# Performance work log

Measured on AMD Instinct MI355X. Metric: run time of the kernel, lower is better.

Reference implementation:

```python
import jax, jax.numpy as jnp
import numpy as np

DIM = 512
DIM_HEAD = 32
HEADS = DIM // DIM_HEAD
WS = 8  # window (partition) size
INNER = (DIM * 4 * 2 // 3 // 32) * 32  # gated-MLP inner dim = 2720
EPS = 1e-6
LS_INIT = 1e-5


def _ln(x, g, b):
    mu = jnp.mean(x, axis=-1, keepdims=True)
    var = jnp.var(x, axis=-1, keepdims=True)
    return (x - mu) * jax.lax.rsqrt(var + EPS) * g + b


def setup_inputs() -> dict:
    key = jax.random.key(0)
    ks = jax.random.split(key, 8)
    B, H, W = 8, 96, 96
    s = lambda d: 1.0 / np.sqrt(d)
    return {
        "x": jax.random.normal(ks[0], (B, H, W, DIM), jnp.float32),
        "norm1_g": jnp.ones((DIM,), jnp.float32),
        "norm1_b": jnp.zeros((DIM,), jnp.float32),
        "qkv_w": jax.random.normal(ks[1], (DIM, 3 * DIM), jnp.float32) * s(DIM),
        "qkv_b": jnp.zeros((3 * DIM,), jnp.float32),
        "proj_w": jax.random.normal(ks[2], (DIM, DIM), jnp.float32) * s(DIM),
        "proj_b": jnp.zeros((DIM,), jnp.float32),
        "ls1": jnp.full((DIM,), LS_INIT, jnp.float32),
        "norm2_g": jnp.ones((DIM,), jnp.float32),
        "norm2_b": jnp.zeros((DIM,), jnp.float32),
        "glu_w": jax.random.normal(ks[3], (DIM, 2 * INNER), jnp.float32) * s(DIM),
        "glu_b": jnp.zeros((2 * INNER,), jnp.float32),
        "fc2_w": jax.random.normal(ks[4], (INNER, DIM), jnp.float32) * s(INNER),
        "fc2_b": jnp.zeros((DIM,), jnp.float32),
        "ls2": jnp.full((DIM,), LS_INIT, jnp.float32),
    }


def reference(x, norm1_g, norm1_b, qkv_w, qkv_b, proj_w, proj_b, ls1,
              norm2_g, norm2_b, glu_w, glu_b, fc2_w, fc2_b, ls2):
    B, H, W, C = x.shape
    nH, nW = H // WS, W // WS
    T = WS * WS  # tokens per window

    # ---- window attention branch ----
    y = _ln(x, norm1_g, norm1_b)
    # window_partition: (B,H,W,C) -> (B*nH*nW, T, C)
    y = y.reshape(B, nH, WS, nW, WS, C).transpose(0, 1, 3, 2, 4, 5)
    y = y.reshape(-1, T, C)
    qkv = y @ qkv_w + qkv_b                      # (M, T, 3C)
    qkv = qkv.reshape(-1, T, 3, HEADS, DIM_HEAD)
    q, k, v = qkv[:, :, 0], qkv[:, :, 1], qkv[:, :, 2]   # (M, T, h, d)
    scale = DIM_HEAD ** -0.5
    attn = jnp.einsum('mqhd,mkhd->mhqk', q, k) * scale
    attn = jax.nn.softmax(attn, axis=-1)
    o = jnp.einsum('mhqk,mkhd->mqhd', attn, v).reshape(-1, T, C)
    o = o @ proj_w + proj_b
    # window_reverse: (M, T, C) -> (B, H, W, C)
    o = o.reshape(B, nH, nW, WS, WS, C).transpose(0, 1, 3, 2, 4, 5)
    o = o.reshape(B, H, W, C)
    x = x + ls1 * o

    # ---- gated MLP branch (GLU with SiLU) ----
    y = _ln(x, norm2_g, norm2_b)
    h = y @ glu_w + glu_b
    h, gate = jnp.split(h, 2, axis=-1)
    h = h * jax.nn.silu(gate)
    h = h @ fc2_w + fc2_b
    x = x + ls2 * h
    return x
```

## Files before the change

### kernel.cpp

```cpp
#include <hip/hip_runtime.h>
#include <hip/hip_bf16.h>
#include <stdint.h>
#include <math.h>

#define DIM 512
#define INNER 1344
#define INNERP 1408

typedef __attribute__((ext_vector_type(8))) short vbf8;
typedef __attribute__((ext_vector_type(4))) float vf4;
typedef __attribute__((ext_vector_type(4))) int v4i;
typedef __attribute__((ext_vector_type(8))) int v8i;

typedef __attribute__((address_space(1))) void as1void;
typedef __attribute__((address_space(3))) void as3void;

union frag8 {
  v8i w;
  v4i h[2];
};

__device__ __forceinline__ unsigned pk4fp8(float a, float b, float c, float d) {
  int v = __builtin_amdgcn_cvt_pk_fp8_f32(a, b, 0, false);
  v = __builtin_amdgcn_cvt_pk_fp8_f32(c, d, v, true);
  return (unsigned)v;
}

__device__ __forceinline__ uint32_t quant4(float v) {
  uint32_t s = (__float_as_uint(v) >> 31) << 3;
  float a = fabsf(v);
  uint32_t m = (a > 0.25f) + (a > 0.75f) + (a > 1.25f) + (a > 1.75f) +
               (a > 2.5f) + (a > 3.5f) + (a > 5.0f);
  return s | m;
}

#define MFMA_M(a, b, c, sb) \
  __builtin_amdgcn_mfma_scale_f32_16x16x128_f8f6f4((a), (b), (c), 0, 4, 0, 127, 0, (sb))

__global__ void k_transpose4(const float* __restrict__ Wsrc, uint8_t* __restrict__ WT,
                             uint8_t* __restrict__ Wsc, int K, int N, int ldB, int ldS,
                             int nsplit) {
  __shared__ float tile[32][33];
  const int tx = threadIdx.x, ty = threadIdx.y;
  const int n0 = blockIdx.x * 32, k0 = blockIdx.y * 32;
#pragma unroll
  for (int i = 0; i < 32; i += 8) {
    int k = k0 + ty + i, n = n0 + tx;
    if (k < K && n < N) tile[ty + i][tx] = Wsrc[(size_t)k * N + n];
  }
  __syncthreads();
  if (tx < 16) {
#pragma unroll
    for (int i = 0; i < 32; i += 8) {
      int n = n0 + ty + i;
      if (n >= N) continue;
      float v0 = tile[2 * tx][ty + i], v1 = tile[2 * tx + 1][ty + i];
      float m = fmaxf(fabsf(v0), fabsf(v1));
      m = fmaxf(m, __shfl_xor(m, 1));
      m = fmaxf(m, __shfl_xor(m, 2));
      m = fmaxf(m, __shfl_xor(m, 4));
      m = fmaxf(m, __shfl_xor(m, 8));
      uint8_t sbyte;
      float s;
      if (m < 1e-20f) {
        sbyte = 0;
        s = 0.0f;
      } else {
        int e = (int)ceilf(log2f(m * 0.166666672f));
        e = e < -126 ? -126 : (e > 126 ? 126 : e);
        sbyte = (uint8_t)(e + 127);
        s = exp2f((float)(-e));
      }
      int np = n + (n >= nsplit ? 64 : 0);
      WT[(size_t)np * ldB + (k0 >> 1) + tx] =
          (uint8_t)(quant4(v0 * s) | (quant4(v1 * s) << 4));
      if (tx == 0) Wsc[(size_t)np * ldS + (k0 >> 5)] = sbyte;
    }
  }
}

__global__ void k_padbias(const float* __restrict__ b, float* __restrict__ o) {
  int c = blockIdx.x * 256 + threadIdx.x;
  if (c < INNER) o[c] = b[c];
  else if (c >= INNERP && c < INNERP + INNER) o[c] = b[c - 64];
  else if (c < 2816) o[c] = 0.0f;
}

template <bool PART, bool BF16IN>
__global__ __launch_bounds__(256) void k_ln(const void* __restrict__ xin,
                                            const float* __restrict__ gw,
                                            const float* __restrict__ bw,
                                            uint8_t* __restrict__ y) {
  const int wave = threadIdx.x >> 6, lane = threadIdx.x & 63;
  const int tok = blockIdx.x * 4 + wave;
  float vals[8];
  if (BF16IN) {
    const __hip_bfloat16* xr = (const __hip_bfloat16*)xin + (size_t)tok * DIM + lane * 8;
    union {
      vbf8 v;
      ushort e[8];
    } u;
    u.v = *(const vbf8*)xr;
#pragma unroll
    for (int j = 0; j < 8; ++j) vals[j] = __uint_as_float((unsigned)u.e[j] << 16);
  } else {
    const float* xr = (const float*)xin + (size_t)tok * DIM + lane * 8;
    const float4 v0 = *(const float4*)xr;
    const float4 v1 = *(const float4*)(xr + 4);
    vals[0] = v0.x; vals[1] = v0.y; vals[2] = v0.z; vals[3] = v0.w;
    vals[4] = v1.x; vals[5] = v1.y; vals[6] = v1.z; vals[7] = v1.w;
  }
  float s = 0.f, ss = 0.f;
#pragma unroll
  for (int j = 0; j < 8; ++j) {
    s += vals[j];
    ss += vals[j] * vals[j];
  }
#pragma unroll
  for (int off = 32; off > 0; off >>= 1) {
    s += __shfl_xor(s, off);
    ss += __shfl_xor(ss, off);
  }
  const float mu = s * (1.0f / DIM);
  const float rs = rsqrtf(ss * (1.0f / DIM) - mu * mu + 1e-6f);
  size_t orow;
  if (PART) {
    int b = tok / 9216, rem = tok % 9216;
    int h = rem / 96, w = rem % 96;
    orow = (size_t)(((b * 12 + (h >> 3)) * 12 + (w >> 3)) * 64 + (h & 7) * 8 + (w & 7));
  } else {
    orow = (size_t)tok;
  }
  const float4 g0 = *(const float4*)(gw + lane * 8);
  const float4 g1 = *(const float4*)(gw + lane * 8 + 4);
  const float4 b0 = *(const float4*)(bw + lane * 8);
  const float4 b1 = *(const float4*)(bw + lane * 8 + 4);
  const float gg[8] = {g0.x, g0.y, g0.z, g0.w, g1.x, g1.y, g1.z, g1.w};
  const float bb[8] = {b0.x, b0.y, b0.z, b0.w, b1.x, b1.y, b1.z, b1.w};
  float r[8];
#pragma unroll
  for (int j = 0; j < 8; ++j) r[j] = (vals[j] - mu) * rs * gg[j] + bb[j];
  uint2 po;
  po.x = pk4fp8(r[0], r[1], r[2], r[3]);
  po.y = pk4fp8(r[4], r[5], r[6], r[7]);
  *(uint2*)(y + orow * DIM + lane * 8) = po;
}

template <int ROWS>
__device__ __forceinline__ void stage8(const uint8_t* __restrict__ g, int ldKb, char* lds,
                                       int wave, int lane) {
  constexpr int RPW = ROWS / 4;
  const int r0 = wave * RPW;
  const int ro = lane >> 3;
  const int pb = lane & 7;
  const uint8_t* src = g + (size_t)(r0 + ro) * (size_t)ldKb + ((pb ^ ro) << 4);
  char* dst = lds + r0 * 128;
#pragma unroll
  for (int c = 0; c < RPW; c += 8)
    __builtin_amdgcn_global_load_lds((const as1void*)(src + (size_t)c * (size_t)ldKb),
                                     (as3void*)(dst + c * 128), 16, 0, 0);
}
__device__ __forceinline__ v8i fragA8(const char* base, int row, int g) {
  const int ro = row & 7;
  const v4i lo = *(const v4i*)(base + row * 128 + (((2 * g) ^ ro) << 4));
  const v4i hi = *(const v4i*)(base + row * 128 + (((2 * g + 1) ^ ro) << 4));
  return __builtin_shufflevector(lo, hi, 0, 1, 2, 3, 4, 5, 6, 7);
}

template <int ROWS>
__device__ __forceinline__ void stage4(const uint8_t* __restrict__ g, int ldKb, char* lds,
                                       int wave, int lane) {
  constexpr int RPW = ROWS / 4;
  const int r0 = wave * RPW;
  const int srw = lane >> 2, sbk = lane & 3;
  const int fsw = (srw + (srw >> 2)) & 3;
  const uint8_t* src = g + (size_t)(r0 + srw) * (size_t)ldKb + ((sbk ^ fsw) << 4);
  char* dst = lds + r0 * 64;
#pragma unroll
  for (int c = 0; c < RPW; c += 16)
    __builtin_amdgcn_global_load_lds((const as1void*)(src + (size_t)c * (size_t)ldKb),
                                     (as3void*)(dst + c * 64), 16, 0, 0);
}
__device__ __forceinline__ v4i fragB4(const char* base, int row, int g) {
  const int f = (row + (row >> 2)) & 3;
  return *(const v4i*)(base + row * 64 + ((g ^ f) << 4));
}

template <int MODE, int NT>
__global__ __launch_bounds__(256, 2) void k_gemm_m(const uint8_t* __restrict__ A8,
                                                   const uint8_t* __restrict__ B4,
                                                   const uint8_t* __restrict__ Bsc,
                                                   const float* __restrict__ bias,
                                                   void* __restrict__ outp,
                                                   const void* __restrict__ resid,
                                                   const float* __restrict__ lsv, const int K,
                                                   const int ldOut) {
  __shared__ alignas(16) char As[128 * 128];
  __shared__ alignas(16) char Bs[128 * 64];
  const int nwg = gridDim.x;
  int bid = blockIdx.x;
  bid = (bid & 7) * (nwg >> 3) + (bid >> 3);
  const int bm = bid / NT, bn = bid % NT;
  const int tid = threadIdx.x, wave = tid >> 6, lane = tid & 63;
  const int wr = wave >> 1, wc = wave & 1;
  const int cl = lane & 15, g = lane >> 4;
  const int KB = K >> 5, nkt = K >> 7;

  const uint8_t* Ab = A8 + (size_t)bm * 128 * K;
  const uint8_t* Bb = B4 + (size_t)bn * 128 * (K >> 1);

  const uint8_t* bscp[4];
#pragma unroll
  for (int i = 0; i < 4; ++i)
    bscp[i] = Bsc + (size_t)(bn * 128 + wc * 64 + cl + i * 16) * KB + g;

  frag8 bfr[4];
#pragma unroll
  for (int i = 0; i < 4; ++i) bfr[i].w = (v8i){0, 0, 0, 0, 0, 0, 0, 0};
  vf4 acc[4][4] = {};

  for (int t = 0; t < nkt; ++t) {
    __syncthreads();
    stage8<128>(Ab + t * 128, K, As, wave, lane);
    stage4<128>(Bb + t * 64, K >> 1, Bs, wave, lane);
    __syncthreads();
    int sb[4];
#pragma unroll
    for (int i = 0; i < 4; ++i) sb[i] = (int)bscp[i][t * 4];
    v8i af[4];
#pragma unroll
    for (int i = 0; i < 4; ++i) {
      af[i] = fragA8(As, wr * 64 + cl + i * 16, g);
      bfr[i].h[0] = fragB4(Bs, wc * 64 + cl + i * 16, g);
    }
#pragma unroll
    for (int mi = 0; mi < 4; ++mi)
#pragma unroll
      for (int ni = 0; ni < 4; ++ni)
        acc[mi][ni] = MFMA_M(af[mi], bfr[ni].w, acc[mi][ni], sb[ni]);
  }

  const int rl = g << 2;
  const int rbase = bm * 128 + wr * 64;
  const int cbase = bn * 128 + wc * 64;
#pragma unroll
  for (int mi = 0; mi < 4; ++mi) {
#pragma unroll
    for (int j = 0; j < 4; ++j) {
      const int r = rbase + mi * 16 + rl + j;
      size_t orow;
      if (MODE == 1) {
        int m = r >> 6, t = r & 63;
        int b = m / 144, mm = m % 144;
        int wh = mm / 12, ww = mm % 12;
        int h = wh * 8 + (t >> 3), w = ww * 8 + (t & 7);
        orow = (size_t)((b * 96 + h) * 96 + w);
      } else {
        orow = (size_t)r;
      }
#pragma unroll
      for (int ni = 0; ni < 4; ++ni) {
        const int c = cbase + ni * 16 + cl;
        const float v = acc[mi][ni][j] + bias[c];
        if (MODE == 0) {
          ((__hip_bfloat16*)outp)[(size_t)r * ldOut + c] = __float2bfloat16(v);
        } else if (MODE == 1) {
          const float* rx = (const float*)resid;
          ((__hip_bfloat16*)outp)[orow * DIM + c] =
              __float2bfloat16(rx[orow * DIM + c] + lsv[c] * v);
        } else {
          const __hip_bfloat16* rx = (const __hip_bfloat16*)resid;
          ((float*)outp)[(size_t)r * DIM + c] =
              __bfloat162float(rx[(size_t)r * DIM + c]) + lsv[c] * v;
        }
      }
    }
  }
}

__global__ __launch_bounds__(256, 2) void k_gemm_glu_m(const uint8_t* __restrict__ A8,
                                                       const uint8_t* __restrict__ B4,
                                                       const uint8_t* __restrict__ Bsc,
                                                       const float* __restrict__ bias,
                                                       uint8_t* __restrict__ hout) {
  __shared__ alignas(16) char As[128 * 128];
  __shared__ alignas(16) char B0s[64 * 64];
  __shared__ alignas(16) char B1s[64 * 64];
  const int K = DIM, KB = 16;
  const int nwg = gridDim.x;
  int bid = blockIdx.x;
  bid = (bid & 7) * (nwg >> 3) + (bid >> 3);
  const int bm = bid / 22, bn = bid % 22;
  const int tid = threadIdx.x, wave = tid >> 6, lane = tid & 63;
  const int wr = wave >> 1, wc = wave & 1;
  const int cl = lane & 15, g = lane >> 4;

  const uint8_t* Ab = A8 + (size_t)bm * 128 * K;
  const uint8_t* Bb0 = B4 + (size_t)(bn * 64) * 256;
  const uint8_t* Bb1 = B4 + (size_t)(INNERP + bn * 64) * 256;

  const uint8_t* b0scp[2];
  const uint8_t* b1scp[2];
#pragma unroll
  for (int i = 0; i < 2; ++i) {
    int rb = wc * 32 + cl + i * 16;
    b0scp[i] = Bsc + (size_t)(bn * 64 + rb) * KB + g;
    b1scp[i] = Bsc + (size_t)(INNERP + bn * 64 + rb) * KB + g;
  }

  frag8 b0f[2], b1f[2];
#pragma unroll
  for (int i = 0; i < 2; ++i) {
    b0f[i].w = (v8i){0, 0, 0, 0, 0, 0, 0, 0};
    b1f[i].w = (v8i){0, 0, 0, 0, 0, 0, 0, 0};
  }
  vf4 a0[4][2] = {}, a1[4][2] = {};

#pragma unroll
  for (int t = 0; t < 4; ++t) {
    __syncthreads();
    stage8<128>(Ab + t * 128, K, As, wave, lane);
    stage4<64>(Bb0 + t * 64, 256, B0s, wave, lane);
    stage4<64>(Bb1 + t * 64, 256, B1s, wave, lane);
    __syncthreads();
    int sb0[2], sb1[2];
#pragma unroll
    for (int i = 0; i < 2; ++i) {
      sb0[i] = (int)b0scp[i][t * 4];
      sb1[i] = (int)b1scp[i][t * 4];
    }
    v8i af[4];
#pragma unroll
    for (int i = 0; i < 4; ++i) af[i] = fragA8(As, wr * 64 + cl + i * 16, g);
#pragma unroll
    for (int i = 0; i < 2; ++i) {
      b0f[i].h[0] = fragB4(B0s, wc * 32 + cl + i * 16, g);
      b1f[i].h[0] = fragB4(B1s, wc * 32 + cl + i * 16, g);
    }
#pragma unroll
    for (int mi = 0; mi < 4; ++mi)
#pragma unroll
      for (int ni = 0; ni < 2; ++ni) {
        a0[mi][ni] = MFMA_M(af[mi], b0f[ni].w, a0[mi][ni], sb0[ni]);
        a1[mi][ni] = MFMA_M(af[mi], b1f[ni].w, a1[mi][ni], sb1[ni]);
      }
  }

  const int rl = g << 2;
  const int rbase = bm * 128 + wr * 64;
  const int cbase = bn * 64 + wc * 32;
#pragma unroll
  for (int mi = 0; mi < 4; ++mi)
#pragma unroll
    for (int j = 0; j < 4; ++j) {
      const int r = rbase + mi * 16 + rl + j;
#pragma unroll
      for (int ni = 0; ni < 2; ++ni) {
        const int c = cbase + ni * 16 + cl;
        const float a = a0[mi][ni][j] + bias[c];
        const float gv = a1[mi][ni][j] + bias[INNERP + c];
        const float sg = 1.0f / (1.0f + __expf(-gv));
        const float hv = a * gv * sg;
        hout[(size_t)r * INNERP + c] =
            (uint8_t)(__builtin_amdgcn_cvt_pk_fp8_f32(hv, hv, 0, false) & 0xff);
      }
    }
}

__global__ __launch_bounds__(256, 2) void k_attn_mfma(const __hip_bfloat16* __restrict__ qkv,
                                                      uint8_t* __restrict__ o) {
  __shared__ __hip_bfloat16 sm[4][6912];
  const int wave = threadIdx.x >> 6, lane = threadIdx.x & 63;
  const int task = blockIdx.x * 4 + wave;
  const int w = task >> 4, hd = task & 15;
  const int g = lane >> 4, c = lane & 15;
  __hip_bfloat16* smp = sm[wave];
  __hip_bfloat16* smv = smp + 4608;

  const __hip_bfloat16* base = qkv + (size_t)w * 64 * 1536 + hd * 32;

  vbf8 qf[4], kf[4];
#pragma unroll
  for (int i = 0; i < 4; ++i) {
    const __hip_bfloat16* qrow = base + (size_t)(i * 16 + c) * 1536 + g * 8;
    qf[i] = *(const vbf8*)qrow;
    kf[i] = *(const vbf8*)(qrow + 512);
  }

  {
    const __hip_bfloat16* vrow = base + (size_t)lane * 1536 + 1024;
    union {
      vbf8 v;
      ushort e[8];
    } uv[4];
#pragma unroll
    for (int i = 0; i < 4; ++i) uv[i].v = *(const vbf8*)(vrow + i * 8);
#pragma unroll
    for (int d = 0; d < 32; ++d)
      ((ushort*)smv)[d * 72 + lane] = uv[d >> 3].e[d & 7];
  }

  vf4 st[4][4];
#pragma unroll
  for (int iq = 0; iq < 4; ++iq)
#pragma unroll
    for (int it = 0; it < 4; ++it) {
      vf4 z = {};
      st[iq][it] = __builtin_amdgcn_mfma_f32_16x16x32_bf16(qf[iq], kf[it], z, 0, 0, 0);
    }

  float inv[4][4];
#pragma unroll
  for (int iq = 0; iq < 4; ++iq) {
#pragma unroll
    for (int j = 0; j < 4; ++j) {
      float m = fmaxf(fmaxf(st[iq][0][j], st[iq][1][j]), fmaxf(st[iq][2][j], st[iq][3][j]));
      m = fmaxf(m, __shfl_xor(m, 1));
      m = fmaxf(m, __shfl_xor(m, 2));
      m = fmaxf(m, __shfl_xor(m, 4));
      m = fmaxf(m, __shfl_xor(m, 8));
      float s = 0.f;
#pragma unroll
      for (int it = 0; it < 4; ++it) {
        const float e = __expf((st[iq][it][j] - m) * 0.17677669529663687f);
        st[iq][it][j] = e;
        s += e;
      }
      s += __shfl_xor(s, 1);
      s += __shfl_xor(s, 2);
      s += __shfl_xor(s, 4);
      s += __shfl_xor(s, 8);
      inv[iq][j] = 1.0f / s;
    }
  }

#pragma unroll
  for (int iq = 0; iq < 4; ++iq)
#pragma unroll
    for (int j = 0; j < 4; ++j) {
      const int q = iq * 16 + g * 4 + j;
#pragma unroll
      for (int it = 0; it < 4; ++it)
        smp[q * 72 + it * 16 + c] = __float2bfloat16(st[iq][it][j]);
    }

  vf4 ot[4][2] = {};
#pragma unroll
  for (int ks = 0; ks < 2; ++ks) {
    vbf8 pf[4], vfr[2];
#pragma unroll
    for (int iq = 0; iq < 4; ++iq)
      pf[iq] = *(const vbf8*)(smp + (iq * 16 + c) * 72 + ks * 32 + g * 8);
#pragma unroll
    for (int dt = 0; dt < 2; ++dt)
      vfr[dt] = *(const vbf8*)(smv + (dt * 16 + c) * 72 + ks * 32 + g * 8);
#pragma unroll
    for (int iq = 0; iq < 4; ++iq)
#pragma unroll
      for (int dt = 0; dt < 2; ++dt)
        ot[iq][dt] = __builtin_amdgcn_mfma_f32_16x16x32_bf16(pf[iq], vfr[dt], ot[iq][dt], 0, 0, 0);
  }

#pragma unroll
  for (int iq = 0; iq < 4; ++iq)
#pragma unroll
    for (int dt = 0; dt < 2; ++dt)
#pragma unroll
      for (int j = 0; j < 4; ++j) {
        const int q = iq * 16 + g * 4 + j;
        smp[q * 72 + dt * 16 + c] = __float2bfloat16(ot[iq][dt][j] * inv[iq][j]);
      }
  uint8_t* ob = o + (size_t)w * 64 * 512 + hd * 32;
#pragma unroll
  for (int i = 0; i < 4; ++i) {
    const int idx = i * 64 + lane;
    const int row = idx >> 2, chunk = idx & 3;
    union {
      vbf8 v;
      ushort e[8];
    } u;
    u.v = *(const vbf8*)(smp + row * 72 + chunk * 8);
    float f[8];
#pragma unroll
    for (int j = 0; j < 8; ++j) f[j] = __uint_as_float((unsigned)u.e[j] << 16);
    uint2 pv;
    pv.x = pk4fp8(f[0], f[1], f[2], f[3]);
    pv.y = pk4fp8(f[4], f[5], f[6], f[7]);
    *(uint2*)(ob + (size_t)row * 512 + chunk * 8) = pv;
  }
}

extern "C" void kernel_launch(void* const* d_in, const int* in_sizes, int n_in, void* d_out,
                              int out_size, void* d_ws, size_t ws_size, hipStream_t stream) {
  const float* x = (const float*)d_in[0];
  const float* n1g = (const float*)d_in[1];
  const float* n1b = (const float*)d_in[2];
  const float* qkv_w = (const float*)d_in[3];
  const float* qkv_b = (const float*)d_in[4];
  const float* proj_w = (const float*)d_in[5];
  const float* proj_b = (const float*)d_in[6];
  const float* ls1 = (const float*)d_in[7];
  const float* n2g = (const float*)d_in[8];
  const float* n2b = (const float*)d_in[9];
  const float* glu_w = (const float*)d_in[10];
  const float* glu_b = (const float*)d_in[11];
  const float* fc2_w = (const float*)d_in[12];
  const float* fc2_b = (const float*)d_in[13];
  const float* ls2 = (const float*)d_in[14];

  if (ws_size < 268000000u) return;

  char* ws = (char*)d_ws;
  uint8_t* wTq4 = (uint8_t*)(ws + 0);
  uint8_t* wTp4 = (uint8_t*)(ws + 393216);
  uint8_t* wTg4 = (uint8_t*)(ws + 524288);
  uint8_t* wTf4 = (uint8_t*)(ws + 1245184);
  uint8_t* sq = (uint8_t*)(ws + 1605632);
  uint8_t* sp = (uint8_t*)(ws + 1630208);
  uint8_t* sg = (uint8_t*)(ws + 1638400);
  uint8_t* sf = (uint8_t*)(ws + 1683456);
  float* gbias = (float*)(ws + 1705984);
  uint8_t* act8 = (uint8_t*)(ws + 2097152);
  char* big = ws + 39845888;
  __hip_bfloat16* qkvbuf = (__hip_bfloat16*)big;
  uint8_t* h8 = (uint8_t*)big;
  __hip_bfloat16* x1b = (__hip_bfloat16*)(big + 109051904);

  hipMemsetAsync(wTg4, 0, 720896, stream);
  hipMemsetAsync(wTf4, 0, 360448, stream);
  hipMemsetAsync(sg, 0, 45056, stream);
  hipMemsetAsync(sf, 0, 22528, stream);

  dim3 tb(32, 8);
  k_transpose4<<<dim3(48, 16), tb, 0, stream>>>(qkv_w, wTq4, sq, 512, 1536, 256, 16, 1 << 30);
  k_transpose4<<<dim3(16, 16), tb, 0, stream>>>(proj_w, wTp4, sp, 512, 512, 256, 16, 1 << 30);
  k_transpose4<<<dim3(84, 16), tb, 0, stream>>>(glu_w, wTg4, sg, 512, 2688, 256, 16, INNER);
  k_transpose4<<<dim3(16, 42), tb, 0, stream>>>(fc2_w, wTf4, sf, 1344, 512, 704, 44, 1 << 30);
  k_padbias<<<11, 256, 0, stream>>>(glu_b, gbias);

  k_ln<true, false><<<18432, 256, 0, stream>>>(x, n1g, n1b, act8);
  k_gemm_m<0, 12><<<6912, 256, 0, stream>>>(act8, wTq4, sq, qkv_b, qkvbuf, nullptr, nullptr, 512, 1536);
  k_attn_mfma<<<4608, 256, 0, stream>>>(qkvbuf, act8);
  k_gemm_m<1, 4><<<2304, 256, 0, stream>>>(act8, wTp4, sp, proj_b, (void*)x1b, x, ls1, 512, 512);
  k_ln<false, true><<<18432, 256, 0, stream>>>(x1b, n2g, n2b, act8);
  k_gemm_glu_m<<<12672, 256, 0, stream>>>(act8, wTg4, sg, gbias, h8);
  k_gemm_m<2, 4><<<2304, 256, 0, stream>>>(h8, wTf4, sf, fc2_b, d_out, x1b, ls2, INNERP, 512);
}
```

Before: 570.1 us.

## Swap MFMA operands for vectorized epilogue stores and prefetch block scales

Result: slower. 591.7 us (+3.8%).

```diff
diff --git a/kernel.cpp b/kernel.cpp
--- a/kernel.cpp
+++ b/kernel.cpp
@@ -34,8 +34,8 @@
   return s | m;
 }
 
-#define MFMA_M(a, b, c, sb) \
-  __builtin_amdgcn_mfma_scale_f32_16x16x128_f8f6f4((a), (b), (c), 0, 4, 0, 127, 0, (sb))
+#define MFMA_W(w, a, c, sb) \
+  __builtin_amdgcn_mfma_scale_f32_16x16x128_f8f6f4((w), (a), (c), 4, 0, 0, (sb), 0, 127)
 
 __global__ void k_transpose4(const float* __restrict__ Wsrc, uint8_t* __restrict__ WT,
                              uint8_t* __restrict__ Wsc, int K, int N, int ldB, int ldS,
@@ -187,7 +187,7 @@
 }
 
 template <int MODE, int NT>
-__global__ __launch_bounds__(256, 2) void k_gemm_m(const uint8_t* __restrict__ A8,
+__global__ __launch_bounds__(256, 3) void k_gemm_m(const uint8_t* __restrict__ A8,
                                                    const uint8_t* __restrict__ B4,
                                                    const uint8_t* __restrict__ Bsc,
                                                    const float* __restrict__ bias,
@@ -219,14 +219,20 @@
   for (int i = 0; i < 4; ++i) bfr[i].w = (v8i){0, 0, 0, 0, 0, 0, 0, 0};
   vf4 acc[4][4] = {};
 
+  int sb[4];
+#pragma unroll
+  for (int i = 0; i < 4; ++i) sb[i] = (int)bscp[i][0];
+
   for (int t = 0; t < nkt; ++t) {
     __syncthreads();
     stage8<128>(Ab + t * 128, K, As, wave, lane);
     stage4<128>(Bb + t * 64, K >> 1, Bs, wave, lane);
+    int sbn[4] = {};
+    if (t + 1 < nkt) {
+#pragma unroll
+      for (int i = 0; i < 4; ++i) sbn[i] = (int)bscp[i][(t + 1) * 4];
+    }
     __syncthreads();
-    int sb[4];
-#pragma unroll
-    for (int i = 0; i < 4; ++i) sb[i] = (int)bscp[i][t * 4];
     v8i af[4];
 #pragma unroll
     for (int i = 0; i < 4; ++i) {
@@ -237,48 +243,107 @@
     for (int mi = 0; mi < 4; ++mi)
 #pragma unroll
       for (int ni = 0; ni < 4; ++ni)
-        acc[mi][ni] = MFMA_M(af[mi], bfr[ni].w, acc[mi][ni], sb[ni]);
-  }
-
-  const int rl = g << 2;
+        acc[mi][ni] = MFMA_W(bfr[ni].w, af[mi], acc[mi][ni], sb[ni]);
+#pragma unroll
+    for (int i = 0; i < 4; ++i) sb[i] = sbn[i];
+  }
+
   const int rbase = bm * 128 + wr * 64;
   const int cbase = bn * 128 + wc * 64;
-#pragma unroll
-  for (int mi = 0; mi < 4; ++mi) {
-#pragma unroll
-    for (int j = 0; j < 4; ++j) {
-      const int r = rbase + mi * 16 + rl + j;
-      size_t orow;
-      if (MODE == 1) {
-        int m = r >> 6, t = r & 63;
-        int b = m / 144, mm = m % 144;
-        int wh = mm / 12, ww = mm % 12;
-        int h = wh * 8 + (t >> 3), w = ww * 8 + (t & 7);
-        orow = (size_t)((b * 96 + h) * 96 + w);
-      } else {
-        orow = (size_t)r;
-      }
+  const int c4 = cbase + g * 4;
+
+  if (MODE == 0) {
+    float4 bz[4];
+#pragma unroll
+    for (int ni = 0; ni < 4; ++ni) bz[ni] = *(const float4*)(bias + c4 + ni * 16);
+    __hip_bfloat16* ob = (__hip_bfloat16*)outp;
+#pragma unroll
+    for (int mi = 0; mi < 4; ++mi) {
+      const int r = rbase + mi * 16 + cl;
+      __hip_bfloat16* op = ob + (size_t)r * ldOut + c4;
 #pragma unroll
       for (int ni = 0; ni < 4; ++ni) {
-        const int c = cbase + ni * 16 + cl;
-        const float v = acc[mi][ni][j] + bias[c];
-        if (MODE == 0) {
-          ((__hip_bfloat16*)outp)[(size_t)r * ldOut + c] = __float2bfloat16(v);
-        } else if (MODE == 1) {
-          const float* rx = (const float*)resid;
-          ((__hip_bfloat16*)outp)[orow * DIM + c] =
-              __float2bfloat16(rx[orow * DIM + c] + lsv[c] * v);
-        } else {
-          const __hip_bfloat16* rx = (const __hip_bfloat16*)resid;
-          ((float*)outp)[(size_t)r * DIM + c] =
-              __bfloat162float(rx[(size_t)r * DIM + c]) + lsv[c] * v;
-        }
-      }
-    }
-  }
-}
-
-__global__ __launch_bounds__(256, 2) void k_gemm_glu_m(const uint8_t* __restrict__ A8,
+        const float* bzp = &bz[ni].x;
+        union {
+          uint2 u;
+          __hip_bfloat16 b[4];
+        } pk;
+#pragma unroll
+        for (int j = 0; j < 4; ++j) pk.b[j] = __float2bfloat16(acc[mi][ni][j] + bzp[j]);
+        *(uint2*)(op + ni * 16) = pk.u;
+      }
+    }
+  } else if (MODE == 1) {
+    float4 bz[4], lz[4];
+#pragma unroll
+    for (int ni = 0; ni < 4; ++ni) {
+      bz[ni] = *(const float4*)(bias + c4 + ni * 16);
+      lz[ni] = *(const float4*)(lsv + c4 + ni * 16);
+    }
+    __hip_bfloat16* ob = (__hip_bfloat16*)outp;
+    const float* rx = (const float*)resid;
+#pragma unroll
+    for (int mi = 0; mi < 4; ++mi) {
+      const int r = rbase + mi * 16 + cl;
+      int mwin = r >> 6, t2 = r & 63;
+      int b = mwin / 144, mm = mwin % 144;
+      int wh = mm / 12, ww = mm % 12;
+      int h = wh * 8 + (t2 >> 3), w = ww * 8 + (t2 & 7);
+      size_t orow = (size_t)((b * 96 + h) * 96 + w);
+      const float* rxp = rx + orow * DIM + c4;
+      __hip_bfloat16* op = ob + orow * DIM + c4;
+#pragma unroll
+      for (int ni = 0; ni < 4; ++ni) {
+        const float4 rv = *(const float4*)(rxp + ni * 16);
+        const float* rvp = &rv.x;
+        const float* bzp = &bz[ni].x;
+        const float* lzp = &lz[ni].x;
+        union {
+          uint2 u;
+          __hip_bfloat16 b[4];
+        } pk;
+#pragma unroll
+        for (int j = 0; j < 4; ++j)
+          pk.b[j] = __float2bfloat16(rvp[j] + lzp[j] * (acc[mi][ni][j] + bzp[j]));
+        *(uint2*)(op + ni * 16) = pk.u;
+      }
+    }
+  } else {
+    float4 bz[4], lz[4];
+#pragma unroll
+    for (int ni = 0; ni < 4; ++ni) {
+      bz[ni] = *(const float4*)(bias + c4 + ni * 16);
+      lz[ni] = *(const float4*)(lsv + c4 + ni * 16);
+    }
+    float* of = (float*)outp;
+    const __hip_bfloat16* rx = (const __hip_bfloat16*)resid;
+#pragma unroll
+    for (int mi = 0; mi < 4; ++mi) {
+      const int r = rbase + mi * 16 + cl;
+      const __hip_bfloat16* rxp = rx + (size_t)r * DIM + c4;
+      float* op = of + (size_t)r * DIM + c4;
+#pragma unroll
+      for (int ni = 0; ni < 4; ++ni) {
+        union {
+          uint2 u;
+          ushort s[4];
+        } rr;
+        rr.u = *(const uint2*)(rxp + ni * 16);
+        const float* bzp = &bz[ni].x;
+        const float* lzp = &lz[ni].x;
+        float4 o;
+        float* opv = &o.x;
+#pragma unroll
+        for (int j = 0; j < 4; ++j)
+          opv[j] = __uint_as_float((unsigned)rr.s[j] << 16) +
+                   lzp[j] * (acc[mi][ni][j] + bzp[j]);
+        *(float4*)(op + ni * 16) = o;
+      }
+    }
+  }
+}
+
+__global__ __launch_bounds__(256, 3) void k_gemm_glu_m(const uint8_t* __restrict__ A8,
                                                        const uint8_t* __restrict__ B4,
                                                        const uint8_t* __restrict__ Bsc,
                                                        const float* __restrict__ bias,
@@ -316,19 +381,28 @@
   }
   vf4 a0[4][2] = {}, a1[4][2] = {};
 
+  int sb0[2], sb1[2];
+#pragma unroll
+  for (int i = 0; i < 2; ++i) {
+    sb0[i] = (int)b0scp[i][0];
+    sb1[i] = (int)b1scp[i][0];
+  }
+
 #pragma unroll
   for (int t = 0; t < 4; ++t) {
     __syncthreads();
     stage8<128>(Ab + t * 128, K, As, wave, lane);
     stage4<64>(Bb0 + t * 64, 256, B0s, wave, lane);
     stage4<64>(Bb1 + t * 64, 256, B1s, wave, lane);
+    int sn0[2] = {}, sn1[2] = {};
+    if (t < 3) {
+#pragma unroll
+      for (int i = 0; i < 2; ++i) {
+        sn0[i] = (int)b0scp[i][(t + 1) * 4];
+        sn1[i] = (int)b1scp[i][(t + 1) * 4];
+      }
+    }
     __syncthreads();
-    int sb0[2], sb1[2];
-#pragma unroll
-    for (int i = 0; i < 2; ++i) {
-      sb0[i] = (int)b0scp[i][t * 4];
-      sb1[i] = (int)b1scp[i][t * 4];
-    }
     v8i af[4];
 #pragma unroll
     for (int i = 0; i < 4; ++i) af[i] = fragA8(As, wr * 64 + cl + i * 16, g);
@@ -341,30 +415,44 @@
     for (int mi = 0; mi < 4; ++mi)
 #pragma unroll
       for (int ni = 0; ni < 2; ++ni) {
-        a0[mi][ni] = MFMA_M(af[mi], b0f[ni].w, a0[mi][ni], sb0[ni]);
-        a1[mi][ni] = MFMA_M(af[mi], b1f[ni].w, a1[mi][ni], sb1[ni]);
-      }
-  }
-
-  const int rl = g << 2;
+        a0[mi][ni] = MFMA_W(b0f[ni].w, af[mi], a0[mi][ni], sb0[ni]);
+        a1[mi][ni] = MFMA_W(b1f[ni].w, af[mi], a1[mi][ni], sb1[ni]);
+      }
+#pragma unroll
+    for (int i = 0; i < 2; ++i) {
+      sb0[i] = sn0[i];
+      sb1[i] = sn1[i];
+    }
+  }
+
   const int rbase = bm * 128 + wr * 64;
   const int cbase = bn * 64 + wc * 32;
-#pragma unroll
-  for (int mi = 0; mi < 4; ++mi)
-#pragma unroll
-    for (int j = 0; j < 4; ++j) {
-      const int r = rbase + mi * 16 + rl + j;
-#pragma unroll
-      for (int ni = 0; ni < 2; ++ni) {
-        const int c = cbase + ni * 16 + cl;
-        const float a = a0[mi][ni][j] + bias[c];
-        const float gv = a1[mi][ni][j] + bias[INNERP + c];
+  const int c4 = cbase + g * 4;
+  float4 bh[2], bg[2];
+#pragma unroll
+  for (int ni = 0; ni < 2; ++ni) {
+    bh[ni] = *(const float4*)(bias + c4 + ni * 16);
+    bg[ni] = *(const float4*)(bias + INNERP + c4 + ni * 16);
+  }
+#pragma unroll
+  for (int mi = 0; mi < 4; ++mi) {
+    const int r = rbase + mi * 16 + cl;
+    uint8_t* hp = hout + (size_t)r * INNERP + c4;
+#pragma unroll
+    for (int ni = 0; ni < 2; ++ni) {
+      const float* bhp = &bh[ni].x;
+      const float* bgp = &bg[ni].x;
+      float hv[4];
+#pragma unroll
+      for (int j = 0; j < 4; ++j) {
+        const float a = a0[mi][ni][j] + bhp[j];
+        const float gv = a1[mi][ni][j] + bgp[j];
         const float sg = 1.0f / (1.0f + __expf(-gv));
-        const float hv = a * gv * sg;
-        hout[(size_t)r * INNERP + c] =
-            (uint8_t)(__builtin_amdgcn_cvt_pk_fp8_f32(hv, hv, 0, false) & 0xff);
-      }
-    }
+        hv[j] = a * gv * sg;
+      }
+      *(uint32_t*)(hp + ni * 16) = pk4fp8(hv[0], hv[1], hv[2], hv[3]);
+    }
+  }
 }
 
 __global__ __launch_bounds__(256, 2) void k_attn_mfma(const __hip_bfloat16* __restrict__ qkv,
```
